# Performance work log

Hardware: AMD Instinct MI355X
Metric: run time of the kernel (lower is better)

Reference implementation:

```python
import jax, jax.numpy as jnp
import numpy as np
import math

V, BS, D, L, H = 50257, 1024, 768, 12, 4
DH = D // H  # 192
B, T = 4, 1024


def setup_inputs() -> dict:
    key = jax.random.key(0)
    ks = jax.random.split(key, 18)
    s = 0.02
    inp = {
        "x": jax.random.randint(ks[0], (B, T), 0, V),
        "tok_emb": jax.random.normal(ks[1], (V, D), jnp.float32) * s,
        "pos_emb": jax.random.normal(ks[2], (BS, D), jnp.float32) * s,
        "ln1_s": jnp.ones((L, D), jnp.float32),
        "ln1_b": jnp.zeros((L, D), jnp.float32),
        "qkv_w": jax.random.normal(ks[3], (L, D, 3 * D), jnp.float32) * s,
        "qkv_b": jnp.zeros((L, 3 * D), jnp.float32),
        "ln2_s": jnp.ones((L, D), jnp.float32),
        "ln2_b": jnp.zeros((L, D), jnp.float32),
        "fc_w": jax.random.normal(ks[4], (L, D, 4 * D), jnp.float32) * s,
        "fc_b": jnp.zeros((L, 4 * D), jnp.float32),
        "proj_w": jax.random.normal(ks[5], (L, 4 * D, D), jnp.float32) * s,
        "proj_b": jnp.zeros((L, D), jnp.float32),
        "lnf_s": jnp.ones((D,), jnp.float32),
        "lnf_b": jnp.zeros((D,), jnp.float32),
        "head_w": jax.random.normal(ks[6], (D, V), jnp.float32) * s,
        "head_b": jnp.zeros((V,), jnp.float32),
    }
    return inp


def _ln(x, scale, shift):
    m = x.mean(-1, keepdims=True)
    v = jnp.mean((x - m) ** 2, axis=-1, keepdims=True)
    return (x - m) * jax.lax.rsqrt(v + 1e-5) * scale + shift


def _forward(x, tok_emb, pos_emb, ln1_s, ln1_b, qkv_w, qkv_b, ln2_s, ln2_b,
             fc_w, fc_b, proj_w, proj_b, lnf_s, lnf_b, head_w, head_b):
    Bx, Tx = x.shape
    h = tok_emb[x] + pos_emb[:Tx]  # [B,T,D]
    causal = jnp.tril(jnp.ones((Tx, Tx), bool))
    scale = 1.0 / math.sqrt(DH)

    def block(h, p):
        s1, b1, wq, bq, s2, b2, wf, bf, wp, bp = p
        # attention (no output projection, faithful to source)
        ln1 = _ln(h, s1, b1)
        qkv = ln1 @ wq + bq  # [B,T,3D]
        q, k, v = jnp.split(qkv, 3, axis=-1)
        q = q.reshape(Bx, Tx, H, DH)
        k = k.reshape(Bx, Tx, H, DH)
        v = v.reshape(Bx, Tx, H, DH)
        att = jnp.einsum('bthd,bshd->bhts', q, k) * scale
        att = jnp.where(causal, att, -jnp.inf)
        att = jax.nn.softmax(att, axis=-1)
        y = jnp.einsum('bhts,bshd->bthd', att, v).reshape(Bx, Tx, D)
        h = h + y
        # MLP (ReLU, despite attr named gelu in source)
        ln2 = _ln(h, s2, b2)
        m = jax.nn.relu(ln2 @ wf + bf) @ wp + bp
        return h + m, None

    h, _ = jax.lax.scan(block, h,
                        (ln1_s, ln1_b, qkv_w, qkv_b, ln2_s, ln2_b,
                         fc_w, fc_b, proj_w, proj_b))
    h = _ln(h, lnf_s, lnf_b)
    return h @ head_w + head_b  # [B,T,V]


def reference(x, tok_emb, pos_emb, ln1_s, ln1_b, qkv_w, qkv_b, ln2_s, ln2_b,
              fc_w, fc_b, proj_w, proj_b, lnf_s, lnf_b, head_w, head_b):
    return _forward(x, tok_emb, pos_emb, ln1_s, ln1_b, qkv_w, qkv_b,
                    ln2_s, ln2_b, fc_w, fc_b, proj_w, proj_b,
                    lnf_s, lnf_b, head_w, head_b)
```

## Files before the change

### kernel.cpp

```cpp
#include <hip/hip_runtime.h>
#include <stdint.h>

#define D_MODEL 768
#define NHEAD 4
#define DHEAD 192
#define SEQ 1024
#define NLAYER 12
#define NTOK 4096
#define NVOCAB 50257

typedef __attribute__((ext_vector_type(4))) float f32x4;
typedef __attribute__((ext_vector_type(4))) int i32x4;
typedef __attribute__((ext_vector_type(4))) unsigned short u16x4;

__device__ __forceinline__ unsigned short f2bf(float f) {
  unsigned u = __builtin_bit_cast(unsigned, f);
  u += 0x7FFFu + ((u >> 16) & 1u);
  return (unsigned short)(u >> 16);
}

#define GLDS(src, dst)                                                   \
  __builtin_amdgcn_global_load_lds(                                      \
      (const __attribute__((address_space(1))) void*)(src),              \
      (__attribute__((address_space(3))) void*)(dst), 16, 0, 0)

__global__ __launch_bounds__(256) void embed_kernel(
    const int* __restrict__ x, const float* __restrict__ tok,
    const float* __restrict__ pos, float* __restrict__ h) {
  int row = blockIdx.x;
  int t = row & (SEQ - 1);
  int id = x[row];
  const float* tp = tok + (long)id * D_MODEL;
  const float* pp = pos + (long)t * D_MODEL;
  float* hp = h + (long)row * D_MODEL;
  for (int j = threadIdx.x; j < D_MODEL; j += 256)
    hp[j] = tp[j] + pp[j];
}

__global__ __launch_bounds__(256) void ln_kernel(
    const float* __restrict__ h, const float* __restrict__ sc,
    const float* __restrict__ sh, unsigned short* __restrict__ out) {
  __shared__ float red[4];
  int row = blockIdx.x;
  const float* x = h + (long)row * D_MODEL;
  int tid = threadIdx.x;
  float v0 = x[tid], v1 = x[tid + 256], v2 = x[tid + 512];
  float s = v0 + v1 + v2;
  for (int o = 32; o > 0; o >>= 1) s += __shfl_xor(s, o);
  if ((tid & 63) == 0) red[tid >> 6] = s;
  __syncthreads();
  float mean = (red[0] + red[1] + red[2] + red[3]) * (1.0f / D_MODEL);
  __syncthreads();
  float d0 = v0 - mean, d1 = v1 - mean, d2 = v2 - mean;
  float q = d0 * d0 + d1 * d1 + d2 * d2;
  for (int o = 32; o > 0; o >>= 1) q += __shfl_xor(q, o);
  if ((tid & 63) == 0) red[tid >> 6] = q;
  __syncthreads();
  float var = (red[0] + red[1] + red[2] + red[3]) * (1.0f / D_MODEL);
  float r = rsqrtf(var + 1e-5f);
  unsigned short* op = out + (long)row * D_MODEL;
  op[tid]       = f2bf(d0 * r * sc[tid]       + sh[tid]);
  op[tid + 256] = f2bf(d1 * r * sc[tid + 256] + sh[tid + 256]);
  op[tid + 512] = f2bf(d2 * r * sc[tid + 512] + sh[tid + 512]);
}

__global__ __launch_bounds__(256) void wtrans3_kernel(
    const float* __restrict__ qw, const float* __restrict__ fw,
    const float* __restrict__ pw, unsigned short* __restrict__ tq,
    unsigned short* __restrict__ tf, unsigned short* __restrict__ tp) {
  __shared__ unsigned short tile[32][33];
  int bid = blockIdx.x;
  const float* src; unsigned short* dst; int K, N, nb;
  if (bid < 1728)               { src = qw; dst = tq; K = 768;  N = 2304; nb = 72; }
  else if ((bid -= 1728) < 2304){ src = fw; dst = tf; K = 768;  N = 3072; nb = 96; }
  else { bid -= 2304;             src = pw; dst = tp; K = 3072; N = 768;  nb = 24; }
  int n0 = (bid % nb) * 32, k0 = (bid / nb) * 32;
  int tx = threadIdx.x & 31, ty = threadIdx.x >> 5;
  #pragma unroll
  for (int i = 0; i < 4; ++i) {
    int k = k0 + ty + i * 8;
    tile[ty + i * 8][tx] = f2bf(src[(long)k * N + n0 + tx]);
  }
  __syncthreads();
  #pragma unroll
  for (int i = 0; i < 4; ++i) {
    int nn = n0 + ty + i * 8;
    dst[(long)nn * K + k0 + tx] = tile[tx][ty + i * 8];
  }
}

__global__ __launch_bounds__(256) void wtrans_kernel(
    const float* __restrict__ w, unsigned short* __restrict__ wt, int K, int N) {
  __shared__ unsigned short tile[32][33];
  int n0 = blockIdx.x * 32, k0 = blockIdx.y * 32;
  int tx = threadIdx.x, ty = threadIdx.y;
  int n = n0 + tx; if (n >= N) n = N - 1;
  #pragma unroll
  for (int i = 0; i < 4; ++i) {
    int k = k0 + ty + i * 8;
    tile[ty + i * 8][tx] = f2bf(w[(long)k * N + n]);
  }
  __syncthreads();
  #pragma unroll
  for (int i = 0; i < 4; ++i) {
    int nn = n0 + ty + i * 8;
    if (nn < N) wt[(long)nn * K + k0 + tx] = tile[tx][ty + i * 8];
  }
}

__global__ __launch_bounds__(256) void vt_kernel(
    const unsigned short* __restrict__ qkv, unsigned short* __restrict__ vt) {
  __shared__ unsigned short tile[32][33];
  int bh = blockIdx.z, b = bh >> 2, hh = bh & 3;
  int t0 = blockIdx.x * 32, f0 = blockIdx.y * 32;
  int tx = threadIdx.x, ty = threadIdx.y;
  const unsigned short* src = qkv + (long)b * SEQ * 2304 + 2 * D_MODEL + hh * DHEAD;
  #pragma unroll
  for (int i = 0; i < 4; ++i) {
    int t = t0 + ty + i * 8;
    tile[ty + i * 8][tx] = src[(long)t * 2304 + f0 + tx];
  }
  __syncthreads();
  unsigned short* dst = vt + (long)bh * DHEAD * SEQ;
  #pragma unroll
  for (int i = 0; i < 4; ++i) {
    int f = f0 + ty + i * 8;
    dst[(long)f * SEQ + t0 + tx] = tile[tx][ty + i * 8];
  }
}

__global__ __launch_bounds__(256) void softmax_kernel(
    const float* __restrict__ S, unsigned short* __restrict__ P) {
  __shared__ float red[4];
  long rid = blockIdx.x;
  int q = (int)(rid & (SEQ - 1));
  int tid = threadIdx.x;
  int i0 = tid * 4;
  f32x4 v;
  if (i0 <= q) {
    v = *(const f32x4*)(S + rid * SEQ + i0);
  } else {
    v = f32x4{-3.0e38f, -3.0e38f, -3.0e38f, -3.0e38f};
  }
  float m = -3.0e38f;
  #pragma unroll
  for (int j = 0; j < 4; ++j) {
    if (i0 + j > q) v[j] = -3.0e38f;
    m = fmaxf(m, v[j]);
  }
  for (int o = 32; o > 0; o >>= 1) m = fmaxf(m, __shfl_xor(m, o));
  if ((tid & 63) == 0) red[tid >> 6] = m;
  __syncthreads();
  m = fmaxf(fmaxf(red[0], red[1]), fmaxf(red[2], red[3]));
  __syncthreads();
  float e[4];
  float sum = 0.f;
  #pragma unroll
  for (int j = 0; j < 4; ++j) {
    e[j] = (i0 + j > q) ? 0.f : __expf(v[j] - m);
    sum += e[j];
  }
  for (int o = 32; o > 0; o >>= 1) sum += __shfl_xor(sum, o);
  if ((tid & 63) == 0) red[tid >> 6] = sum;
  __syncthreads();
  float inv = 1.0f / (red[0] + red[1] + red[2] + red[3]);
  if ((i0 >> 7) <= (q >> 7)) {
    u16x4 out;
    #pragma unroll
    for (int j = 0; j < 4; ++j) out[j] = f2bf(e[j] * inv);
    *(u16x4*)(P + rid * SEQ + i0) = out;
  }
}

#define BM 128
#define BN 128
#define BKK 32

template<int MODE>
__global__ __launch_bounds__(256) void gemm_kernel(
    const unsigned short* __restrict__ A, int lda,
    const unsigned short* __restrict__ B, int ldb,
    const float* __restrict__ bias,
    void* __restrict__ Cv, int ldc,
    int M, int N, int K,
    int NI, long sAo, long sAi, long sBo, long sBi,
    long sCo, long sCi, float alpha, int causal, int mblocks) {
  __shared__ __align__(16) unsigned short As[BM * BKK];
  __shared__ __align__(16) unsigned short Bs[BN * BKK];
  int z = blockIdx.z;
  int zo = z / NI, zi = z - zo * NI;
  A += zo * sAo + zi * sAi;
  B += zo * sBo + zi * sBi;
  long coff = zo * sCo + zi * sCi;

  int m0, n0;
  if (mblocks > 0) {
    int bid = blockIdx.x;
    int qq = (int)gridDim.x >> 3;
    bid = (bid & 7) * qq + (bid >> 3);
    m0 = (bid % mblocks) * BM;
    n0 = (bid / mblocks) * BN;
  } else {
    m0 = blockIdx.y * BM;
    n0 = blockIdx.x * BN;
  }
  if (causal == 1 && n0 > m0 + BM - 1) return;
  int kmax = (causal == 2) ? min(K, m0 + BM) : K;

  int tid = threadIdx.x;
  int lane = tid & 63;
  int wave = tid >> 6;
  int wm = (wave >> 1) * 64;
  int wn = (wave & 1) * 64;

  f32x4 acc[4][4] = {};

  for (int k0 = 0; k0 < kmax; k0 += BKK) {
    __syncthreads();
    #pragma unroll
    for (int i = 0; i < 2; ++i) {
      int c0 = i * 256 + wave * 64;
      int cc = c0 + lane;
      int row = cc >> 2;
      int ko = (cc & 3) << 3;
      GLDS(A + (long)(m0 + row) * lda + k0 + ko, As + c0 * 8);
      int rg = n0 + row; if (rg >= N) rg = N - 1;
      GLDS(B + (long)rg * ldb + k0 + ko, Bs + c0 * 8);
    }
    __syncthreads();
    int lr = lane & 15;
    int kg = (lane >> 4) << 3;
    i32x4 af[4], bf[4];
    #pragma unroll
    for (int mi = 0; mi < 4; ++mi)
      af[mi] = *(const i32x4*)(As + (wm + mi * 16 + lr) * BKK + kg);
    #pragma unroll
    for (int ni = 0; ni < 4; ++ni)
      bf[ni] = *(const i32x4*)(Bs + (wn + ni * 16 + lr) * BKK + kg);
    #pragma unroll
    for (int mi = 0; mi < 4; ++mi)
      #pragma unroll
      for (int ni = 0; ni < 4; ++ni)
        asm("v_mfma_f32_16x16x32_bf16 %0, %1, %2, %0"
            : "+v"(acc[mi][ni]) : "v"(bf[ni]), "v"(af[mi]));
  }

  int cm = lane & 15;
  int cg = (lane >> 4) << 2;
  #pragma unroll
  for (int mi = 0; mi < 4; ++mi) {
    long row = m0 + wm + mi * 16 + cm;
    #pragma unroll
    for (int ni = 0; ni < 4; ++ni) {
      int col = n0 + wn + ni * 16 + cg;
      f32x4 v = acc[mi][ni];
      if (MODE == 2) {
        #pragma unroll
        for (int r = 0; r < 4; ++r) v[r] *= alpha;
        *(f32x4*)((float*)Cv + coff + row * (long)ldc + col) = v;
      } else if (MODE == 0 || MODE == 1) {
        f32x4 bv = *(const f32x4*)(bias + col);
        u16x4 o;
        #pragma unroll
        for (int r = 0; r < 4; ++r) {
          float t = v[r] + bv[r];
          if (MODE == 1) t = fmaxf(t, 0.f);
          o[r] = f2bf(t);
        }
        *(u16x4*)((unsigned short*)Cv + coff + row * (long)ldc + col) = o;
      } else {
        float* cp = (float*)Cv + coff + row * (long)ldc + col;
        if (col + 4 <= N) {
          f32x4 bv = bias ? *(const f32x4*)(bias + col)
                          : f32x4{0.f, 0.f, 0.f, 0.f};
          if (MODE == 3) {
            f32x4 old = *(f32x4*)cp;
            #pragma unroll
            for (int r = 0; r < 4; ++r) old[r] += v[r] + bv[r];
            *(f32x4*)cp = old;
          } else {
            f32x4 o;
            #pragma unroll
            for (int r = 0; r < 4; ++r) o[r] = v[r] + bv[r];
            *(f32x4*)cp = o;
          }
        } else {
          #pragma unroll
          for (int r = 0; r < 4; ++r) {
            if (col + r < N) {
              float bvr = bias ? bias[col + r] : 0.f;
              if (MODE == 3) cp[r] += v[r] + bvr;
              else           cp[r] = v[r] + bvr;
            }
          }
        }
      }
    }
  }
}

extern "C" void kernel_launch(void* const* d_in, const int* in_sizes, int n_in,
                              void* d_out, int out_size, void* d_ws, size_t ws_size,
                              hipStream_t stream) {
  const int*   x       = (const int*)  d_in[0];
  const float* tok_emb = (const float*)d_in[1];
  const float* pos_emb = (const float*)d_in[2];
  const float* ln1_s   = (const float*)d_in[3];
  const float* ln1_b   = (const float*)d_in[4];
  const float* qkv_w   = (const float*)d_in[5];
  const float* qkv_b   = (const float*)d_in[6];
  const float* ln2_s   = (const float*)d_in[7];
  const float* ln2_b   = (const float*)d_in[8];
  const float* fc_w    = (const float*)d_in[9];
  const float* fc_b    = (const float*)d_in[10];
  const float* proj_w  = (const float*)d_in[11];
  const float* proj_b  = (const float*)d_in[12];
  const float* lnf_s   = (const float*)d_in[13];
  const float* lnf_b   = (const float*)d_in[14];
  const float* head_w  = (const float*)d_in[15];
  const float* head_b  = (const float*)d_in[16];

  char* ws = (char*)d_ws;
  size_t off = 0;
  auto alloc = [&](size_t bytes) {
    char* p = ws + off;
    off += (bytes + 255) & ~(size_t)255;
    return p;
  };
  float*          h   = (float*)         alloc((size_t)NTOK * D_MODEL * 4);
  unsigned short* lnb = (unsigned short*)alloc((size_t)NTOK * D_MODEL * 2);
  unsigned short* qkv = (unsigned short*)alloc((size_t)NTOK * 2304 * 2);
  unsigned short* vt  = (unsigned short*)alloc((size_t)16 * DHEAD * SEQ * 2);
  unsigned short* mid = (unsigned short*)alloc((size_t)NTOK * 3072 * 2);
  float*          S   = (float*)         alloc((size_t)16 * SEQ * SEQ * 4);
  unsigned short* P   = (unsigned short*)alloc((size_t)16 * SEQ * SEQ * 2);
  unsigned short* wtq = (unsigned short*)alloc((size_t)2304 * 768 * 2);
  unsigned short* wtf = (unsigned short*)alloc((size_t)3072 * 768 * 2);
  unsigned short* wtp = (unsigned short*)alloc((size_t)768 * 3072 * 2);
  unsigned short* wth = (unsigned short*)alloc((size_t)50304 * 768 * 2);

  embed_kernel<<<NTOK, 256, 0, stream>>>(x, tok_emb, pos_emb, h);

  const float rscale = 0.07216878364870323f;

  for (int l = 0; l < NLAYER; ++l) {
    wtrans3_kernel<<<6336, 256, 0, stream>>>(
        qkv_w + (long)l * 768 * 2304, fc_w + (long)l * 768 * 3072,
        proj_w + (long)l * 3072 * 768, wtq, wtf, wtp);
    ln_kernel<<<NTOK, 256, 0, stream>>>(h, ln1_s + l * 768, ln1_b + l * 768, lnb);
    gemm_kernel<0><<<dim3(18, 32, 1), 256, 0, stream>>>(
        lnb, 768, wtq, 768, qkv_b + l * 2304, qkv, 2304,
        4096, 2304, 768, 1, 0, 0, 0, 0, 0, 0, 1.0f, 0, 0);
    vt_kernel<<<dim3(32, 6, 16), dim3(32, 8), 0, stream>>>(qkv, vt);
    gemm_kernel<2><<<dim3(8, 8, 16), 256, 0, stream>>>(
        qkv, 2304, qkv + 768, 2304, nullptr, S, 1024,
        1024, 1024, 192, 4,
        (long)1024 * 2304, 192, (long)1024 * 2304, 192,
        (long)4 * 1024 * 1024, (long)1024 * 1024, rscale, 1, 0);
    softmax_kernel<<<16384, 256, 0, stream>>>(S, P);
    gemm_kernel<3><<<dim3(2, 8, 16), 256, 0, stream>>>(
        P, 1024, vt, 1024, nullptr, h, 768,
        1024, 192, 1024, 4,
        (long)4 * 1024 * 1024, (long)1024 * 1024,
        (long)4 * 192 * 1024, (long)192 * 1024,
        (long)1024 * 768, 192, 1.0f, 2, 0);
    ln_kernel<<<NTOK, 256, 0, stream>>>(h, ln2_s + l * 768, ln2_b + l * 768, lnb);
    gemm_kernel<1><<<dim3(24, 32, 1), 256, 0, stream>>>(
        lnb, 768, wtf, 768, fc_b + l * 3072, mid, 3072,
        4096, 3072, 768, 1, 0, 0, 0, 0, 0, 0, 1.0f, 0, 0);
    gemm_kernel<3><<<dim3(6, 32, 1), 256, 0, stream>>>(
        mid, 3072, wtp, 3072, proj_b + l * 768, h, 768,
        4096, 768, 3072, 1, 0, 0, 0, 0, 0, 0, 1.0f, 0, 0);
  }

  wtrans_kernel<<<dim3(1571, 24), dim3(32, 8), 0, stream>>>(head_w, wth, 768, 50257);
  ln_kernel<<<NTOK, 256, 0, stream>>>(h, lnf_s, lnf_b, lnb);
  gemm_kernel<4><<<dim3(393 * 32, 1, 1), 256, 0, stream>>>(
      lnb, 768, wth, 768, head_b, (float*)d_out, 50257,
      4096, 50257, 768, 1, 0, 0, 0, 0, 0, 0, 1.0f, 0, 32);
}
```

Before: 3.355 ms.

## Double-buffer GEMM LDS tiles and remap XCD block swizzle for head GEMM

The GEMM kernel now keeps two LDS buffers for the A and B tiles. It issues the async global-to-LDS loads for the next K tile before running the MFMAs on the current tile, which cuts one barrier per iteration and overlaps memory with compute. Separately, the swizzled block mapping used by the vocab-head GEMM now gives each XCD a fixed band of M-blocks and walks across N. This changes the L2 reuse pattern: A rows stay local, but every XCD may stream the whole head weight. LDS use per block doubles to 32KB, which could reduce occupancy.

```diff
diff --git a/kernel.cpp b/kernel.cpp
--- a/kernel.cpp
+++ b/kernel.cpp
@@ -185,8 +185,8 @@
     int M, int N, int K,
     int NI, long sAo, long sAi, long sBo, long sBi,
     long sCo, long sCi, float alpha, int causal, int mblocks) {
-  __shared__ __align__(16) unsigned short As[BM * BKK];
-  __shared__ __align__(16) unsigned short Bs[BN * BKK];
+  __shared__ __align__(16) unsigned short As[2][BM * BKK];
+  __shared__ __align__(16) unsigned short Bs[2][BN * BKK];
   int z = blockIdx.z;
   int zo = z / NI, zi = z - zo * NI;
   A += zo * sAo + zi * sAi;
@@ -196,10 +196,11 @@
   int m0, n0;
   if (mblocks > 0) {
     int bid = blockIdx.x;
-    int qq = (int)gridDim.x >> 3;
-    bid = (bid & 7) * qq + (bid >> 3);
-    m0 = (bid % mblocks) * BM;
-    n0 = (bid / mblocks) * BN;
+    int mpx = mblocks >> 3;
+    int xcd = bid & 7;
+    int c = bid >> 3;
+    m0 = (xcd * mpx + (c & (mpx - 1))) * BM;
+    n0 = (c / mpx) * BN;
   } else {
     m0 = blockIdx.y * BM;
     n0 = blockIdx.x * BN;
@@ -213,36 +214,43 @@
   int wm = (wave >> 1) * 64;
   int wn = (wave & 1) * 64;
 
-  f32x4 acc[4][4] = {};
-
-  for (int k0 = 0; k0 < kmax; k0 += BKK) {
-    __syncthreads();
+  auto stage = [&](int buf, int k0) {
     #pragma unroll
     for (int i = 0; i < 2; ++i) {
       int c0 = i * 256 + wave * 64;
       int cc = c0 + lane;
       int row = cc >> 2;
       int ko = (cc & 3) << 3;
-      GLDS(A + (long)(m0 + row) * lda + k0 + ko, As + c0 * 8);
+      GLDS(A + (long)(m0 + row) * lda + k0 + ko, As[buf] + c0 * 8);
       int rg = n0 + row; if (rg >= N) rg = N - 1;
-      GLDS(B + (long)rg * ldb + k0 + ko, Bs + c0 * 8);
+      GLDS(B + (long)rg * ldb + k0 + ko, Bs[buf] + c0 * 8);
     }
-    __syncthreads();
+  };
+
+  f32x4 acc[4][4] = {};
+  int nt = kmax / BKK;
+  stage(0, 0);
+  __syncthreads();
+  int cur = 0;
+  for (int t = 0; t < nt; ++t) {
+    if (t + 1 < nt) stage(cur ^ 1, (t + 1) * BKK);
     int lr = lane & 15;
     int kg = (lane >> 4) << 3;
     i32x4 af[4], bf[4];
     #pragma unroll
     for (int mi = 0; mi < 4; ++mi)
-      af[mi] = *(const i32x4*)(As + (wm + mi * 16 + lr) * BKK + kg);
+      af[mi] = *(const i32x4*)(As[cur] + (wm + mi * 16 + lr) * BKK + kg);
     #pragma unroll
     for (int ni = 0; ni < 4; ++ni)
-      bf[ni] = *(const i32x4*)(Bs + (wn + ni * 16 + lr) * BKK + kg);
+      bf[ni] = *(const i32x4*)(Bs[cur] + (wn + ni * 16 + lr) * BKK + kg);
     #pragma unroll
     for (int mi = 0; mi < 4; ++mi)
       #pragma unroll
       for (int ni = 0; ni < 4; ++ni)
         asm("v_mfma_f32_16x16x32_bf16 %0, %1, %2, %0"
             : "+v"(acc[mi][ni]) : "v"(bf[ni]), "v"(af[mi]));
+    __syncthreads();
+    cur ^= 1;
   }
 
   int cm = lane & 15;
@@ -375,7 +383,7 @@
 
   wtrans_kernel<<<dim3(1571, 24), dim3(32, 8), 0, stream>>>(head_w, wth, 768, 50257);
   ln_kernel<<<NTOK, 256, 0, stream>>>(h, lnf_s, lnf_b, lnb);
-  gemm_kernel<4><<<dim3(393 * 32, 1, 1), 256, 0, stream>>>(
+  gemm_kernel<4><<<dim3(32 * 393, 1, 1), 256, 0, stream>>>(
       lnb, 768, wth, 768, head_b, (float*)d_out, 50257,
       4096, 50257, 768, 1, 0, 0, 0, 0, 0, 0, 1.0f, 0, 32);
 }
```

Result: faster. 3.273 ms (-2.4%).
